# Kernel tuning notes

Hardware: AMD Instinct MI355X
Metric: run time of the kernel (lower is better)

The kernel has to match this reference:

```python
import jax, jax.numpy as jnp
import numpy as np

B, CH, H, W = 1, 128, 160, 224


def _lrelu(x):
    return jax.nn.leaky_relu(x, 0.01)


def _conv(x, w, b):
    # 1x1 conv: x [B,Cin,H,W], w [Cout,Cin], b [Cout]
    return jnp.einsum('bchw,oc->bohw', x, w) + b[None, :, None, None]


def _cmul(x, inds, Wt, b):
    # CondMul: x [N,Cin], inds [N] int32, Wt [classes,Cin,Cout], b [classes,Cout]
    return jnp.einsum('ni,nio->no', x, jnp.take(Wt, inds, axis=0)) + jnp.take(b, inds, axis=0)


def _forward(x_in, bb1_w, bb1_b, bb2_w, bb2_b, bb3_w, bb3_b,
             msk1_w, msk1_b, msk2_w, msk2_b, msk3_w, msk3_b,
             c10_w, c10_b, c20_w, c20_b, c30_w, c30_b,
             c11_W, c11_b, c21_W, c21_b, c31_W, c31_b,
             c12_W, c12_b, c22_W, c22_b, c32_W, c32_b,
             r1_w, r1_b, r2_W, r2_b, r3_W, r3_b):
    Bb, C, Hh, Ww = x_in.shape
    # backbone (1x1 convs)
    x = _lrelu(_conv(x_in, bb1_w, bb1_b))
    x = _lrelu(_conv(x, bb2_w, bb2_b))
    feat = _lrelu(_conv(x, bb3_w, bb3_b))  # [B,128,H,W]
    # mask head (note: torch applies leaky_relu to msk3 output too)
    m = _lrelu(_conv(x_in, msk1_w, msk1_b))
    m = _lrelu(_conv(m, msk2_w, msk2_b))
    mask = _lrelu(_conv(m, msk3_w, msk3_b))  # [B,1,H,W]
    # stage 1: dense classification over classes[0]=16
    y = _lrelu(_conv(feat, c10_w, c10_b))
    y = _lrelu(_conv(y, c20_w, c20_b))
    y = _conv(y, c30_w, c30_b)  # [B,16,H,W], no relu
    inds1 = jnp.argmax(y, axis=1).reshape(-1).astype(jnp.int32)  # [N], (b,h,w) order
    x_l = jnp.transpose(feat, (0, 2, 3, 1)).reshape(-1, feat.shape[1])  # [N,128]
    # stage 2: CondMul routed by inds1 (16 classes), out = 16+2*8 = 32
    t = _lrelu(_cmul(x_l, inds1, c11_W, c11_b))
    t = _lrelu(_cmul(t, inds1, c21_W, c21_b))
    t = _cmul(t, inds1, c31_W, c31_b)
    inds2 = jnp.argmax(t, axis=1).astype(jnp.int32)
    inds12 = jnp.clip(inds1 * 16 + (inds2 - 8), 0, 255).astype(jnp.int32)
    # stage 3: CondMul routed by inds12 (256 classes)
    t = _lrelu(_cmul(x_l, inds12, c12_W, c12_b))
    t = _lrelu(_cmul(t, inds12, c22_W, c22_b))
    t = _cmul(t, inds12, c32_W, c32_b)
    inds3 = jnp.argmax(t, axis=1).astype(jnp.int32)
    inds123 = jnp.clip(inds12 * 16 + (inds3 - 8), 0, 4095).astype(jnp.int32)  # classes123-1
    inds_super = inds123 // 512  # class_factor = 4096/8
    xr = _lrelu(_conv(x_in, r1_w, r1_b))
    xr_l = jnp.transpose(xr, (0, 2, 3, 1)).reshape(-1, xr.shape[1])  # [N,128]
    t = _lrelu(_cmul(xr_l, inds_super, r2_W, r2_b))
    r = _cmul(t, inds123, r3_W, r3_b).reshape(-1)
    out = ((inds123.astype(jnp.float32) + r) * (1.0 / 4096.0)).reshape(Bb, 1, Hh, Ww)
    return out, mask


def setup_inputs():
    ks = jax.random.split(jax.random.key(0), 40)
    ctr = iter(range(40))

    def p(shape, scale=0.05):
        return jax.random.normal(ks[next(ctr)], shape, dtype=jnp.float32) * scale

    d = {
        'x_in': p((B, CH, H, W), 1.0),
        'bb1_w': p((128, 128)), 'bb1_b': p((128,)),
        'bb2_w': p((128, 128)), 'bb2_b': p((128,)),
        'bb3_w': p((128, 128)), 'bb3_b': p((128,)),
        'msk1_w': p((32, 128)), 'msk1_b': p((32,)),
        'msk2_w': p((16, 32)), 'msk2_b': p((16,)),
        'msk3_w': p((1, 16)), 'msk3_b': p((1,)),
        'c10_w': p((32, 128)), 'c10_b': p((32,)),
        'c20_w': p((32, 32)), 'c20_b': p((32,)),
        'c30_w': p((16, 32)), 'c30_b': p((16,)),
        'c11_W': p((16, 128, 32)), 'c11_b': p((16, 32)),
        'c21_W': p((16, 32, 32)), 'c21_b': p((16, 32)),
        'c31_W': p((16, 32, 32)), 'c31_b': p((16, 32)),
        'c12_W': p((256, 128, 32)), 'c12_b': p((256, 32)),
        'c22_W': p((256, 32, 32)), 'c22_b': p((256, 32)),
        'c32_W': p((256, 32, 32)), 'c32_b': p((256, 32)),
        'r1_w': p((128, 128)), 'r1_b': p((128,)),
        'r2_W': p((8, 128, 32)), 'r2_b': p((8, 32)),
        'r3_W': p((4096, 32, 1)), 'r3_b': p((4096, 1)),
    }
    return d


def reference(x_in, bb1_w, bb1_b, bb2_w, bb2_b, bb3_w, bb3_b,
              msk1_w, msk1_b, msk2_w, msk2_b, msk3_w, msk3_b,
              c10_w, c10_b, c20_w, c20_b, c30_w, c30_b,
              c11_W, c11_b, c21_W, c21_b, c31_W, c31_b,
              c12_W, c12_b, c22_W, c22_b, c32_W, c32_b,
              r1_w, r1_b, r2_W, r2_b, r3_W, r3_b):
    return _forward(x_in, bb1_w, bb1_b, bb2_w, bb2_b, bb3_w, bb3_b,
                    msk1_w, msk1_b, msk2_w, msk2_b, msk3_w, msk3_b,
                    c10_w, c10_b, c20_w, c20_b, c30_w, c30_b,
                    c11_W, c11_b, c21_W, c21_b, c31_W, c31_b,
                    c12_W, c12_b, c22_W, c22_b, c32_W, c32_b,
                    r1_w, r1_b, r2_W, r2_b, r3_W, r3_b)
```

## Files before the change

### kernel.cpp

```cpp
#include <hip/hip_runtime.h>

#define N_PIX (160*224)
#define ORDER_CAP (396*256)
#define CHUNK_CAP 512
#define G_S2 156
#define G_S3 396
#define G_RG 148
#define NB   70
#define BCHUNK 512

__device__ __forceinline__ float lrelu(float v) { return v >= 0.f ? v : 0.01f * v; }

template<int CHW>
__global__ __launch_bounds__(512) void dense128_k(const float* __restrict__ in,
    const float* __restrict__ W, const float* __restrict__ b,
    float* __restrict__ out, int N)
{
  __shared__ float Wl[128*128];
  const int tid = threadIdx.x;
#pragma unroll
  for (int k = 0; k < 8; ++k)
    ((float4*)Wl)[k*512 + tid] = ((const float4*)W)[k*512 + tid];
  const int lane = tid & 63;
  const int wv = tid >> 6;
  const int ob = wv * 16;
  const int p0 = blockIdx.x * 128 + lane;
  const int p1 = p0 + 64;
  float acc0[16], acc1[16];
#pragma unroll
  for (int o = 0; o < 16; ++o) { acc0[o] = b[ob + o]; acc1[o] = acc0[o]; }
  __syncthreads();
  const float* x0 = CHW ? (in + p0) : (in + (size_t)p0 * 128);
  const float* x1 = CHW ? (in + p1) : (in + (size_t)p1 * 128);
  for (int c0 = 0; c0 < 128; c0 += 8) {
    float xa[8], xb[8];
    if (CHW) {
#pragma unroll
      for (int k = 0; k < 8; ++k) {
        xa[k] = x0[(size_t)(c0 + k) * N];
        xb[k] = x1[(size_t)(c0 + k) * N];
      }
    } else {
      float4 a0 = *(const float4*)(x0 + c0), a1 = *(const float4*)(x0 + c0 + 4);
      float4 b0 = *(const float4*)(x1 + c0), b1 = *(const float4*)(x1 + c0 + 4);
      xa[0]=a0.x; xa[1]=a0.y; xa[2]=a0.z; xa[3]=a0.w;
      xa[4]=a1.x; xa[5]=a1.y; xa[6]=a1.z; xa[7]=a1.w;
      xb[0]=b0.x; xb[1]=b0.y; xb[2]=b0.z; xb[3]=b0.w;
      xb[4]=b1.x; xb[5]=b1.y; xb[6]=b1.z; xb[7]=b1.w;
    }
#pragma unroll
    for (int o = 0; o < 16; ++o) {
      const float* wr = &Wl[(ob + o)*128 + c0];
      float4 w0 = *(const float4*)wr;
      float4 w1 = *(const float4*)(wr + 4);
      acc0[o] += xa[0]*w0.x + xa[1]*w0.y + xa[2]*w0.z + xa[3]*w0.w
               + xa[4]*w1.x + xa[5]*w1.y + xa[6]*w1.z + xa[7]*w1.w;
      acc1[o] += xb[0]*w0.x + xb[1]*w0.y + xb[2]*w0.z + xb[3]*w0.w
               + xb[4]*w1.x + xb[5]*w1.y + xb[6]*w1.z + xb[7]*w1.w;
    }
  }
  __syncthreads();
  float4* o0 = (float4*)(out + (size_t)p0 * 128 + ob);
  float4* o1 = (float4*)(out + (size_t)p1 * 128 + ob);
#pragma unroll
  for (int q = 0; q < 4; ++q) {
    o0[q] = make_float4(lrelu(acc0[4*q+0]), lrelu(acc0[4*q+1]),
                        lrelu(acc0[4*q+2]), lrelu(acc0[4*q+3]));
    o1[q] = make_float4(lrelu(acc1[4*q+0]), lrelu(acc1[4*q+1]),
                        lrelu(acc1[4*q+2]), lrelu(acc1[4*q+3]));
  }
}

__global__ __launch_bounds__(256) void mask_k(const float* __restrict__ xg,
    const float* __restrict__ W1, const float* __restrict__ b1,
    const float* __restrict__ W2, const float* __restrict__ b2,
    const float* __restrict__ W3, const float* __restrict__ b3,
    float* __restrict__ outm, int N)
{
  __shared__ float W1l[32*128], W2l[16*32], W3l[16];
  const int tid = threadIdx.x;
#pragma unroll
  for (int k = 0; k < 4; ++k)
    ((float4*)W1l)[k*256 + tid] = ((const float4*)W1)[k*256 + tid];
  if (tid < 128) ((float4*)W2l)[tid] = ((const float4*)W2)[tid];
  if (tid < 4)   ((float4*)W3l)[tid] = ((const float4*)W3)[tid];
  __syncthreads();
  const int p = blockIdx.x * 256 + tid;
  float a1[32];
#pragma unroll
  for (int o = 0; o < 32; ++o) a1[o] = b1[o];
  for (int c0 = 0; c0 < 128; c0 += 8) {
    float xs[8];
#pragma unroll
    for (int k = 0; k < 8; ++k) xs[k] = xg[(size_t)(c0 + k) * N + p];
#pragma unroll
    for (int o = 0; o < 32; ++o) {
      const float* wr = &W1l[o*128 + c0];
      float4 w0 = *(const float4*)wr, w1 = *(const float4*)(wr + 4);
      a1[o] += xs[0]*w0.x + xs[1]*w0.y + xs[2]*w0.z + xs[3]*w0.w
             + xs[4]*w1.x + xs[5]*w1.y + xs[6]*w1.z + xs[7]*w1.w;
    }
  }
#pragma unroll
  for (int o = 0; o < 32; ++o) a1[o] = lrelu(a1[o]);
  float a2[16];
#pragma unroll
  for (int o = 0; o < 16; ++o) a2[o] = b2[o];
#pragma unroll
  for (int i = 0; i < 32; i += 4) {
#pragma unroll
    for (int o = 0; o < 16; ++o) {
      float4 w = *(const float4*)&W2l[o*32 + i];
      a2[o] += a1[i]*w.x + a1[i+1]*w.y + a1[i+2]*w.z + a1[i+3]*w.w;
    }
  }
#pragma unroll
  for (int o = 0; o < 16; ++o) a2[o] = lrelu(a2[o]);
  float a3 = b3[0];
#pragma unroll
  for (int i = 0; i < 16; i += 4) {
    float4 w = *(const float4*)&W3l[i];
    a3 += a2[i]*w.x + a2[i+1]*w.y + a2[i+2]*w.z + a2[i+3]*w.w;
  }
  outm[p] = lrelu(a3);
}

__global__ __launch_bounds__(256) void stage1_k(const float* __restrict__ feat,
    const float* __restrict__ W1, const float* __restrict__ b1,
    const float* __restrict__ W2, const float* __restrict__ b2,
    const float* __restrict__ W3, const float* __restrict__ b3,
    int* __restrict__ inds1, int* __restrict__ blkcnt, int N)
{
  __shared__ float W1l[32*128], W2l[32*32], W3l[16*32];
  __shared__ int hist[16];
  const int tid = threadIdx.x;
#pragma unroll
  for (int k = 0; k < 4; ++k)
    ((float4*)W1l)[k*256 + tid] = ((const float4*)W1)[k*256 + tid];
  ((float4*)W2l)[tid] = ((const float4*)W2)[tid];
  if (tid < 128) ((float4*)W3l)[tid] = ((const float4*)W3)[tid];
  if (tid < 16) hist[tid] = 0;
  __syncthreads();
  const int p = blockIdx.x * 256 + tid;
  const float* x = feat + (size_t)p * 128;
  float a1[32];
#pragma unroll
  for (int o = 0; o < 32; ++o) a1[o] = b1[o];
  for (int c0 = 0; c0 < 128; c0 += 8) {
    float4 xa = *(const float4*)(x + c0);
    float4 xb = *(const float4*)(x + c0 + 4);
    float xs[8] = {xa.x, xa.y, xa.z, xa.w, xb.x, xb.y, xb.z, xb.w};
#pragma unroll
    for (int o = 0; o < 32; ++o) {
      const float* wr = &W1l[o*128 + c0];
      float4 w0 = *(const float4*)wr, w1 = *(const float4*)(wr + 4);
      a1[o] += xs[0]*w0.x + xs[1]*w0.y + xs[2]*w0.z + xs[3]*w0.w
             + xs[4]*w1.x + xs[5]*w1.y + xs[6]*w1.z + xs[7]*w1.w;
    }
  }
#pragma unroll
  for (int o = 0; o < 32; ++o) a1[o] = lrelu(a1[o]);
  float a2[32];
#pragma unroll
  for (int o = 0; o < 32; ++o) a2[o] = b2[o];
#pragma unroll
  for (int i = 0; i < 32; i += 4) {
#pragma unroll
    for (int o = 0; o < 32; ++o) {
      float4 w = *(const float4*)&W2l[o*32 + i];
      a2[o] += a1[i]*w.x + a1[i+1]*w.y + a1[i+2]*w.z + a1[i+3]*w.w;
    }
  }
#pragma unroll
  for (int o = 0; o < 32; ++o) a2[o] = lrelu(a2[o]);
  float lg[16];
#pragma unroll
  for (int o = 0; o < 16; ++o) lg[o] = b3[o];
#pragma unroll
  for (int i = 0; i < 32; i += 4) {
#pragma unroll
    for (int o = 0; o < 16; ++o) {
      float4 w = *(const float4*)&W3l[o*32 + i];
      lg[o] += a2[i]*w.x + a2[i+1]*w.y + a2[i+2]*w.z + a2[i+3]*w.w;
    }
  }
  float bv = lg[0]; int bi = 0;
#pragma unroll
  for (int o = 1; o < 16; ++o) if (lg[o] > bv) { bv = lg[o]; bi = o; }
  inds1[p] = bi;
  atomicAdd(&hist[bi], 1);
  __syncthreads();
  if (tid < 16) blkcnt[blockIdx.x * 16 + tid] = hist[tid];
}

__global__ __launch_bounds__(256) void stage23_k(const float* __restrict__ act,
    const float* __restrict__ W1g, const float* __restrict__ b1g,
    const float* __restrict__ W2g, const float* __restrict__ b2g,
    const float* __restrict__ W3g, const float* __restrict__ b3g,
    const int* __restrict__ chunk_class, const int* __restrict__ order,
    const int* __restrict__ offs_this, const int* __restrict__ cnts_this,
    int* __restrict__ out_ind, int hi)
{
  const int cls = chunk_class[blockIdx.x];
  if (cls < 0) return;
  __shared__ float W1l[128*32], W2l[32*32], W3l[32*32];
  __shared__ float b1l[32], b2l[32], b3l[32];
  const int tid = threadIdx.x;
  const float* W1 = W1g + (size_t)cls * 4096;
  const float* W2 = W2g + (size_t)cls * 1024;
  const float* W3 = W3g + (size_t)cls * 1024;
#pragma unroll
  for (int k = 0; k < 4; ++k)
    ((float4*)W1l)[k*256 + tid] = ((const float4*)W1)[k*256 + tid];
  ((float4*)W2l)[tid] = ((const float4*)W2)[tid];
  ((float4*)W3l)[tid] = ((const float4*)W3)[tid];
  if (tid < 32) {
    b1l[tid] = b1g[cls*32 + tid];
    b2l[tid] = b2g[cls*32 + tid];
    b3l[tid] = b3g[cls*32 + tid];
  }
  const int slot = blockIdx.x * 256 + tid;
  const int end = offs_this[cls] + cnts_this[cls];
  __syncthreads();
  if (slot >= end) return;
  const int p = order[slot];
  const float* x = act + (size_t)p * 128;
  float a1[32];
#pragma unroll
  for (int o = 0; o < 32; ++o) a1[o] = b1l[o];
  for (int i0 = 0; i0 < 128; i0 += 8) {
    float4 xa = *(const float4*)(x + i0);
    float4 xb = *(const float4*)(x + i0 + 4);
    float xs[8] = {xa.x, xa.y, xa.z, xa.w, xb.x, xb.y, xb.z, xb.w};
#pragma unroll
    for (int i = 0; i < 8; ++i) {
#pragma unroll
      for (int o4 = 0; o4 < 8; ++o4) {
        float4 w = *(const float4*)&W1l[(i0 + i)*32 + o4*4];
        a1[o4*4+0] += xs[i]*w.x; a1[o4*4+1] += xs[i]*w.y;
        a1[o4*4+2] += xs[i]*w.z; a1[o4*4+3] += xs[i]*w.w;
      }
    }
  }
#pragma unroll
  for (int o = 0; o < 32; ++o) a1[o] = lrelu(a1[o]);
  float a2[32];
#pragma unroll
  for (int o = 0; o < 32; ++o) a2[o] = b2l[o];
#pragma unroll
  for (int i = 0; i < 32; ++i) {
#pragma unroll
    for (int o4 = 0; o4 < 8; ++o4) {
      float4 w = *(const float4*)&W2l[i*32 + o4*4];
      a2[o4*4+0] += a1[i]*w.x; a2[o4*4+1] += a1[i]*w.y;
      a2[o4*4+2] += a1[i]*w.z; a2[o4*4+3] += a1[i]*w.w;
    }
  }
#pragma unroll
  for (int o = 0; o < 32; ++o) a2[o] = lrelu(a2[o]);
  float a3[32];
#pragma unroll
  for (int o = 0; o < 32; ++o) a3[o] = b3l[o];
#pragma unroll
  for (int i = 0; i < 32; ++i) {
#pragma unroll
    for (int o4 = 0; o4 < 8; ++o4) {
      float4 w = *(const float4*)&W3l[i*32 + o4*4];
      a3[o4*4+0] += a2[i]*w.x; a3[o4*4+1] += a2[i]*w.y;
      a3[o4*4+2] += a2[i]*w.z; a3[o4*4+3] += a2[i]*w.w;
    }
  }
  float bv = a3[0]; int bi = 0;
#pragma unroll
  for (int o = 1; o < 32; ++o) if (a3[o] > bv) { bv = a3[o]; bi = o; }
  int v = cls*16 + bi - 8;
  v = v < 0 ? 0 : (v > hi ? hi : v);
  out_ind[p] = v;
}

__global__ __launch_bounds__(256) void reg_k(const float* __restrict__ act,
    const float* __restrict__ W1g, const float* __restrict__ b1g,
    const float* __restrict__ r3W, const float* __restrict__ r3b,
    const int* __restrict__ chunk_class, const int* __restrict__ order,
    const int* __restrict__ offs_this, const int* __restrict__ cnts_this,
    const int* __restrict__ inds123, float* __restrict__ outr)
{
  const int cls = chunk_class[blockIdx.x];
  if (cls < 0) return;
  __shared__ float W1l[128*32], b1l[32];
  const int tid = threadIdx.x;
  const float* W1 = W1g + (size_t)cls * 4096;
#pragma unroll
  for (int k = 0; k < 4; ++k)
    ((float4*)W1l)[k*256 + tid] = ((const float4*)W1)[k*256 + tid];
  if (tid < 32) b1l[tid] = b1g[cls*32 + tid];
  const int slot = blockIdx.x * 256 + tid;
  const int end = offs_this[cls] + cnts_this[cls];
  __syncthreads();
  if (slot >= end) return;
  const int p = order[slot];
  const float* x = act + (size_t)p * 128;
  float a1[32];
#pragma unroll
  for (int o = 0; o < 32; ++o) a1[o] = b1l[o];
  for (int i0 = 0; i0 < 128; i0 += 8) {
    float4 xa = *(const float4*)(x + i0);
    float4 xb = *(const float4*)(x + i0 + 4);
    float xs[8] = {xa.x, xa.y, xa.z, xa.w, xb.x, xb.y, xb.z, xb.w};
#pragma unroll
    for (int i = 0; i < 8; ++i) {
#pragma unroll
      for (int o4 = 0; o4 < 8; ++o4) {
        float4 w = *(const float4*)&W1l[(i0 + i)*32 + o4*4];
        a1[o4*4+0] += xs[i]*w.x; a1[o4*4+1] += xs[i]*w.y;
        a1[o4*4+2] += xs[i]*w.z; a1[o4*4+3] += xs[i]*w.w;
      }
    }
  }
#pragma unroll
  for (int o = 0; o < 32; ++o) a1[o] = lrelu(a1[o]);
  const int ind = inds123[p];
  const float4* rw = (const float4*)(r3W + (size_t)ind * 32);
  float r = r3b[ind];
#pragma unroll
  for (int k = 0; k < 8; ++k) {
    float4 w = rw[k];
    r += a1[4*k+0]*w.x + a1[4*k+1]*w.y + a1[4*k+2]*w.z + a1[4*k+3]*w.w;
  }
  outr[p] = ((float)ind + r) * (1.0f / 4096.0f);
}

__global__ __launch_bounds__(256) void hist_k(const int* __restrict__ ind,
    int* __restrict__ blkcnt, int shift, int C)
{
  __shared__ int h[256];
  const int tid = threadIdx.x, b = blockIdx.x;
  h[tid] = 0;
  __syncthreads();
  const int base = b * BCHUNK;
  atomicAdd(&h[ind[base + tid] >> shift], 1);
  atomicAdd(&h[ind[base + 256 + tid] >> shift], 1);
  __syncthreads();
  if (tid < C) blkcnt[b * C + tid] = h[tid];
}

__global__ __launch_bounds__(256) void scan_k(const int* __restrict__ blkcnt,
    int* __restrict__ blkbase, int* __restrict__ offsets, int* __restrict__ counts,
    int* __restrict__ chunk_class, int C, int fillTo, int nb)
{
  __shared__ int cl[256], ol[256];
  __shared__ int totChunks;
  const int tid = threadIdx.x;
  if (tid < C) {
    int s = 0;
    for (int b = 0; b < nb; ++b) s += blkcnt[b * C + tid];
    cl[tid] = s;
  }
  __syncthreads();
  if (tid == 0) {
    int off = 0;
    for (int c = 0; c < C; ++c) {
      ol[c] = off;
      off += ((cl[c] + 255) >> 8) << 8;
    }
    totChunks = off >> 8;
  }
  __syncthreads();
  if (tid < C) {
    offsets[tid] = ol[tid];
    counts[tid]  = cl[tid];
    int acc = ol[tid];
    for (int b = 0; b < nb; ++b) {
      int v = blkcnt[b * C + tid];
      blkbase[b * C + tid] = acc;
      acc += v;
    }
    const int start = ol[tid] >> 8;
    const int nch = (cl[tid] + 255) >> 8;
    for (int k = 0; k < nch; ++k) chunk_class[start + k] = tid;
  }
  for (int k = totChunks + tid; k < fillTo; k += 256) chunk_class[k] = -1;
}

__global__ __launch_bounds__(256) void scatter_k(const int* __restrict__ ind,
    const int* __restrict__ blkbase, int* __restrict__ order, int shift, int C,
    int chunkpx)
{
  __shared__ int lcur[256], lbase[256];
  const int tid = threadIdx.x, b = blockIdx.x;
  lcur[tid] = 0;
  if (tid < C) lbase[tid] = blkbase[b * C + tid];
  __syncthreads();
  const int base = b * chunkpx;
  for (int r = 0; r < chunkpx; r += 256) {
    const int p = base + r + tid;
    const int c = ind[p] >> shift;
    const int rank = atomicAdd(&lcur[c], 1);
    order[lbase[c] + rank] = p;
  }
}

extern "C" void kernel_launch(void* const* d_in, const int* in_sizes, int n_in,
                              void* d_out, int out_size, void* d_ws, size_t ws_size,
                              hipStream_t stream)
{
  const int N = N_PIX;
  const float* x_in  = (const float*)d_in[0];
  const float* bb1_w = (const float*)d_in[1];  const float* bb1_b = (const float*)d_in[2];
  const float* bb2_w = (const float*)d_in[3];  const float* bb2_b = (const float*)d_in[4];
  const float* bb3_w = (const float*)d_in[5];  const float* bb3_b = (const float*)d_in[6];
  const float* msk1_w= (const float*)d_in[7];  const float* msk1_b= (const float*)d_in[8];
  const float* msk2_w= (const float*)d_in[9];  const float* msk2_b= (const float*)d_in[10];
  const float* msk3_w= (const float*)d_in[11]; const float* msk3_b= (const float*)d_in[12];
  const float* c10_w = (const float*)d_in[13]; const float* c10_b = (const float*)d_in[14];
  const float* c20_w = (const float*)d_in[15]; const float* c20_b = (const float*)d_in[16];
  const float* c30_w = (const float*)d_in[17]; const float* c30_b = (const float*)d_in[18];
  const float* c11_W = (const float*)d_in[19]; const float* c11_b = (const float*)d_in[20];
  const float* c21_W = (const float*)d_in[21]; const float* c21_b = (const float*)d_in[22];
  const float* c31_W = (const float*)d_in[23]; const float* c31_b = (const float*)d_in[24];
  const float* c12_W = (const float*)d_in[25]; const float* c12_b = (const float*)d_in[26];
  const float* c22_W = (const float*)d_in[27]; const float* c22_b = (const float*)d_in[28];
  const float* c32_W = (const float*)d_in[29]; const float* c32_b = (const float*)d_in[30];
  const float* r1_w  = (const float*)d_in[31]; const float* r1_b  = (const float*)d_in[32];
  const float* r2_W  = (const float*)d_in[33]; const float* r2_b  = (const float*)d_in[34];
  const float* r3_W  = (const float*)d_in[35]; const float* r3_b  = (const float*)d_in[36];

  float* act     = (float*)d_ws;
  int*   inds1   = (int*)(act + (size_t)N * 128);
  int*   inds12  = inds1 + N;
  int*   inds123 = inds12 + N;
  int*   counts  = inds123 + N;
  int*   offs    = counts + 256;
  int*   chunk_cls = offs + 256;
  int*   order     = chunk_cls + CHUNK_CAP;
  int*   blkcnt    = order + ORDER_CAP;
  int*   blkbase   = blkcnt + 70*256;

  float* out_reg  = (float*)d_out;
  float* out_mask = out_reg + N;

  const dim3 B(256);
  const dim3 B512(512);
  const int gDense  = N / 128;
  const int gPix256 = N / 256;

  dense128_k<1><<<gDense, B512, 0, stream>>>(x_in, bb1_w, bb1_b, act, N);
  dense128_k<0><<<gDense, B512, 0, stream>>>(act,  bb2_w, bb2_b, act, N);
  dense128_k<0><<<gDense, B512, 0, stream>>>(act,  bb3_w, bb3_b, act, N);

  mask_k<<<gPix256, B, 0, stream>>>(x_in, msk1_w, msk1_b, msk2_w, msk2_b,
                                    msk3_w, msk3_b, out_mask, N);

  stage1_k<<<gPix256, B, 0, stream>>>(act, c10_w, c10_b, c20_w, c20_b,
                                      c30_w, c30_b, inds1, blkcnt, N);

  scan_k<<<1, B, 0, stream>>>(blkcnt, blkbase, offs, counts, chunk_cls, 16, G_S2, 140);
  scatter_k<<<140, B, 0, stream>>>(inds1, blkbase, order, 0, 16, 256);
  stage23_k<<<G_S2, B, 0, stream>>>(act, c11_W, c11_b, c21_W, c21_b, c31_W, c31_b,
                                    chunk_cls, order, offs, counts, inds12, 255);

  hist_k<<<NB, B, 0, stream>>>(inds12, blkcnt, 0, 256);
  scan_k<<<1, B, 0, stream>>>(blkcnt, blkbase, offs, counts, chunk_cls, 256, G_S3, NB);
  scatter_k<<<NB, B, 0, stream>>>(inds12, blkbase, order, 0, 256, BCHUNK);
  stage23_k<<<G_S3, B, 0, stream>>>(act, c12_W, c12_b, c22_W, c22_b, c32_W, c32_b,
                                    chunk_cls, order, offs, counts, inds123, 4095);

  dense128_k<1><<<gDense, B512, 0, stream>>>(x_in, r1_w, r1_b, act, N);

  hist_k<<<NB, B, 0, stream>>>(inds123, blkcnt, 9, 8);
  scan_k<<<1, B, 0, stream>>>(blkcnt, blkbase, offs, counts, chunk_cls, 8, G_RG, NB);
  scatter_k<<<NB, B, 0, stream>>>(inds123, blkbase, order, 9, 8, BCHUNK);
  reg_k<<<G_RG, B, 0, stream>>>(act, r2_W, r2_b, r3_W, r3_b,
                                chunk_cls, order, offs, counts, inds123, out_reg);
}
```

Before: 533.4 us.

## Split dense 1x1 convs across output halves and shrink per-pixel kernel blocks

The dense 128x128 conv kernel is templated on output count so each block computes only 64 output channels, which doubles the grid and halves the shared-memory weight tile. Ping-pong activation buffers are added in the workspace so that the split blocks never read and write the same buffer in place. The mask and stage1 kernels and the first scatter move to 128-thread blocks with twice as many blocks, to fill the GPU better. The cost is that each input activation is now read twice (once per half), and the workspace must be larger; if it is too small, the code falls back to the old 128-output path.

```diff
diff --git a/kernel.cpp b/kernel.cpp
--- a/kernel.cpp
+++ b/kernel.cpp
@@ -11,24 +11,29 @@
 
 __device__ __forceinline__ float lrelu(float v) { return v >= 0.f ? v : 0.01f * v; }
 
-template<int CHW>
+template<int CHW, int OUTS>
 __global__ __launch_bounds__(512) void dense128_k(const float* __restrict__ in,
     const float* __restrict__ W, const float* __restrict__ b,
     float* __restrict__ out, int N)
 {
-  __shared__ float Wl[128*128];
-  const int tid = threadIdx.x;
-#pragma unroll
-  for (int k = 0; k < 8; ++k)
-    ((float4*)Wl)[k*512 + tid] = ((const float4*)W)[k*512 + tid];
+  __shared__ float Wl[OUTS*128];
+  const int tid = threadIdx.x;
+  const int half = (OUTS == 128) ? 0 : (blockIdx.x & 1);
+  const int pblk = (OUTS == 128) ? blockIdx.x : (blockIdx.x >> 1);
+  const float4* Wg = ((const float4*)W) + half * (OUTS * 32);
+#pragma unroll
+  for (int k = 0; k < OUTS*128/2048; ++k)
+    ((float4*)Wl)[k*512 + tid] = Wg[k*512 + tid];
   const int lane = tid & 63;
   const int wv = tid >> 6;
-  const int ob = wv * 16;
-  const int p0 = blockIdx.x * 128 + lane;
+  constexpr int WO = OUTS / 8;
+  const int ob  = wv * WO;
+  const int obg = half * OUTS + ob;
+  const int p0 = pblk * 128 + lane;
   const int p1 = p0 + 64;
-  float acc0[16], acc1[16];
-#pragma unroll
-  for (int o = 0; o < 16; ++o) { acc0[o] = b[ob + o]; acc1[o] = acc0[o]; }
+  float acc0[WO], acc1[WO];
+#pragma unroll
+  for (int o = 0; o < WO; ++o) { acc0[o] = b[obg + o]; acc1[o] = acc0[o]; }
   __syncthreads();
   const float* x0 = CHW ? (in + p0) : (in + (size_t)p0 * 128);
   const float* x1 = CHW ? (in + p1) : (in + (size_t)p1 * 128);
@@ -49,7 +54,7 @@
       xb[4]=b1.x; xb[5]=b1.y; xb[6]=b1.z; xb[7]=b1.w;
     }
 #pragma unroll
-    for (int o = 0; o < 16; ++o) {
+    for (int o = 0; o < WO; ++o) {
       const float* wr = &Wl[(ob + o)*128 + c0];
       float4 w0 = *(const float4*)wr;
       float4 w1 = *(const float4*)(wr + 4);
@@ -60,10 +65,10 @@
     }
   }
   __syncthreads();
-  float4* o0 = (float4*)(out + (size_t)p0 * 128 + ob);
-  float4* o1 = (float4*)(out + (size_t)p1 * 128 + ob);
-#pragma unroll
-  for (int q = 0; q < 4; ++q) {
+  float4* o0 = (float4*)(out + (size_t)p0 * 128 + obg);
+  float4* o1 = (float4*)(out + (size_t)p1 * 128 + obg);
+#pragma unroll
+  for (int q = 0; q < WO/4; ++q) {
     o0[q] = make_float4(lrelu(acc0[4*q+0]), lrelu(acc0[4*q+1]),
                         lrelu(acc0[4*q+2]), lrelu(acc0[4*q+3]));
     o1[q] = make_float4(lrelu(acc1[4*q+0]), lrelu(acc1[4*q+1]),
@@ -71,7 +76,7 @@
   }
 }
 
-__global__ __launch_bounds__(256) void mask_k(const float* __restrict__ xg,
+__global__ __launch_bounds__(128) void mask_k(const float* __restrict__ xg,
     const float* __restrict__ W1, const float* __restrict__ b1,
     const float* __restrict__ W2, const float* __restrict__ b2,
     const float* __restrict__ W3, const float* __restrict__ b3,
@@ -80,12 +85,12 @@
   __shared__ float W1l[32*128], W2l[16*32], W3l[16];
   const int tid = threadIdx.x;
 #pragma unroll
-  for (int k = 0; k < 4; ++k)
-    ((float4*)W1l)[k*256 + tid] = ((const float4*)W1)[k*256 + tid];
-  if (tid < 128) ((float4*)W2l)[tid] = ((const float4*)W2)[tid];
-  if (tid < 4)   ((float4*)W3l)[tid] = ((const float4*)W3)[tid];
-  __syncthreads();
-  const int p = blockIdx.x * 256 + tid;
+  for (int k = 0; k < 8; ++k)
+    ((float4*)W1l)[k*128 + tid] = ((const float4*)W1)[k*128 + tid];
+  ((float4*)W2l)[tid] = ((const float4*)W2)[tid];
+  if (tid < 4) ((float4*)W3l)[tid] = ((const float4*)W3)[tid];
+  __syncthreads();
+  const int p = blockIdx.x * 128 + tid;
   float a1[32];
 #pragma unroll
   for (int o = 0; o < 32; ++o) a1[o] = b1[o];
@@ -125,7 +130,7 @@
   outm[p] = lrelu(a3);
 }
 
-__global__ __launch_bounds__(256) void stage1_k(const float* __restrict__ feat,
+__global__ __launch_bounds__(128) void stage1_k(const float* __restrict__ feat,
     const float* __restrict__ W1, const float* __restrict__ b1,
     const float* __restrict__ W2, const float* __restrict__ b2,
     const float* __restrict__ W3, const float* __restrict__ b3,
@@ -135,13 +140,15 @@
   __shared__ int hist[16];
   const int tid = threadIdx.x;
 #pragma unroll
-  for (int k = 0; k < 4; ++k)
-    ((float4*)W1l)[k*256 + tid] = ((const float4*)W1)[k*256 + tid];
-  ((float4*)W2l)[tid] = ((const float4*)W2)[tid];
-  if (tid < 128) ((float4*)W3l)[tid] = ((const float4*)W3)[tid];
+  for (int k = 0; k < 8; ++k)
+    ((float4*)W1l)[k*128 + tid] = ((const float4*)W1)[k*128 + tid];
+#pragma unroll
+  for (int k = 0; k < 2; ++k)
+    ((float4*)W2l)[k*128 + tid] = ((const float4*)W2)[k*128 + tid];
+  ((float4*)W3l)[tid] = ((const float4*)W3)[tid];
   if (tid < 16) hist[tid] = 0;
   __syncthreads();
-  const int p = blockIdx.x * 256 + tid;
+  const int p = blockIdx.x * 128 + tid;
   const float* x = feat + (size_t)p * 128;
   float a1[32];
 #pragma unroll
@@ -382,18 +389,18 @@
   for (int k = totChunks + tid; k < fillTo; k += 256) chunk_class[k] = -1;
 }
 
-__global__ __launch_bounds__(256) void scatter_k(const int* __restrict__ ind,
+__global__ void scatter_k(const int* __restrict__ ind,
     const int* __restrict__ blkbase, int* __restrict__ order, int shift, int C,
     int chunkpx)
 {
   __shared__ int lcur[256], lbase[256];
   const int tid = threadIdx.x, b = blockIdx.x;
-  lcur[tid] = 0;
+  if (tid < 256) lcur[tid] = 0;
   if (tid < C) lbase[tid] = blkbase[b * C + tid];
   __syncthreads();
   const int base = b * chunkpx;
-  for (int r = 0; r < chunkpx; r += 256) {
-    const int p = base + r + tid;
+  for (int r = tid; r < chunkpx; r += blockDim.x) {
+    const int p = base + r;
     const int c = ind[p] >> shift;
     const int rank = atomicAdd(&lcur[c], 1);
     order[lbase[c] + rank] = p;
@@ -425,8 +432,7 @@
   const float* r2_W  = (const float*)d_in[33]; const float* r2_b  = (const float*)d_in[34];
   const float* r3_W  = (const float*)d_in[35]; const float* r3_b  = (const float*)d_in[36];
 
-  float* act     = (float*)d_ws;
-  int*   inds1   = (int*)(act + (size_t)N * 128);
+  int*   inds1   = (int*)d_ws;
   int*   inds12  = inds1 + N;
   int*   inds123 = inds12 + N;
   int*   counts  = inds123 + N;
@@ -435,27 +441,39 @@
   int*   order     = chunk_cls + CHUNK_CAP;
   int*   blkcnt    = order + ORDER_CAP;
   int*   blkbase   = blkcnt + 70*256;
+  const size_t intWords = 3*(size_t)N + 512 + CHUNK_CAP + ORDER_CAP + 2*70*256;
+  float* act  = (float*)((int*)d_ws + intWords);
+  const size_t need = intWords*4 + 2*(size_t)N*128*4;
+  const bool halved = ws_size >= need;
+  float* act2 = halved ? (act + (size_t)N*128) : act;
 
   float* out_reg  = (float*)d_out;
   float* out_mask = out_reg + N;
 
   const dim3 B(256);
+  const dim3 B128(128);
   const dim3 B512(512);
-  const int gDense  = N / 128;
-  const int gPix256 = N / 256;
-
-  dense128_k<1><<<gDense, B512, 0, stream>>>(x_in, bb1_w, bb1_b, act, N);
-  dense128_k<0><<<gDense, B512, 0, stream>>>(act,  bb2_w, bb2_b, act, N);
-  dense128_k<0><<<gDense, B512, 0, stream>>>(act,  bb3_w, bb3_b, act, N);
-
-  mask_k<<<gPix256, B, 0, stream>>>(x_in, msk1_w, msk1_b, msk2_w, msk2_b,
-                                    msk3_w, msk3_b, out_mask, N);
-
-  stage1_k<<<gPix256, B, 0, stream>>>(act, c10_w, c10_b, c20_w, c20_b,
-                                      c30_w, c30_b, inds1, blkcnt, N);
-
-  scan_k<<<1, B, 0, stream>>>(blkcnt, blkbase, offs, counts, chunk_cls, 16, G_S2, 140);
-  scatter_k<<<140, B, 0, stream>>>(inds1, blkbase, order, 0, 16, 256);
+  const int gPix128 = N / 128;
+  const int gDenseH = 2 * gPix128;
+
+  if (halved) {
+    dense128_k<1,64><<<gDenseH, B512, 0, stream>>>(x_in, bb1_w, bb1_b, act,  N);
+    dense128_k<0,64><<<gDenseH, B512, 0, stream>>>(act,  bb2_w, bb2_b, act2, N);
+    dense128_k<0,64><<<gDenseH, B512, 0, stream>>>(act2, bb3_w, bb3_b, act,  N);
+  } else {
+    dense128_k<1,128><<<gPix128, B512, 0, stream>>>(x_in, bb1_w, bb1_b, act, N);
+    dense128_k<0,128><<<gPix128, B512, 0, stream>>>(act,  bb2_w, bb2_b, act, N);
+    dense128_k<0,128><<<gPix128, B512, 0, stream>>>(act,  bb3_w, bb3_b, act, N);
+  }
+
+  mask_k<<<gPix128, B128, 0, stream>>>(x_in, msk1_w, msk1_b, msk2_w, msk2_b,
+                                       msk3_w, msk3_b, out_mask, N);
+
+  stage1_k<<<gPix128, B128, 0, stream>>>(act, c10_w, c10_b, c20_w, c20_b,
+                                         c30_w, c30_b, inds1, blkcnt, N);
+
+  scan_k<<<1, B, 0, stream>>>(blkcnt, blkbase, offs, counts, chunk_cls, 16, G_S2, 280);
+  scatter_k<<<280, B128, 0, stream>>>(inds1, blkbase, order, 0, 16, 128);
   stage23_k<<<G_S2, B, 0, stream>>>(act, c11_W, c11_b, c21_W, c21_b, c31_W, c31_b,
                                     chunk_cls, order, offs, counts, inds12, 255);
 
@@ -465,11 +483,16 @@
   stage23_k<<<G_S3, B, 0, stream>>>(act, c12_W, c12_b, c22_W, c22_b, c32_W, c32_b,
                                     chunk_cls, order, offs, counts, inds123, 4095);
 
-  dense128_k<1><<<gDense, B512, 0, stream>>>(x_in, r1_w, r1_b, act, N);
+  float* xr = halved ? act2 : act;
+  if (halved) {
+    dense128_k<1,64><<<gDenseH, B512, 0, stream>>>(x_in, r1_w, r1_b, act2, N);
+  } else {
+    dense128_k<1,128><<<gPix128, B512, 0, stream>>>(x_in, r1_w, r1_b, act, N);
+  }
 
   hist_k<<<NB, B, 0, stream>>>(inds123, blkcnt, 9, 8);
   scan_k<<<1, B, 0, stream>>>(blkcnt, blkbase, offs, counts, chunk_cls, 8, G_RG, NB);
   scatter_k<<<NB, B, 0, stream>>>(inds123, blkbase, order, 9, 8, BCHUNK);
-  reg_k<<<G_RG, B, 0, stream>>>(act, r2_W, r2_b, r3_W, r3_b,
+  reg_k<<<G_RG, B, 0, stream>>>(xr, r2_W, r2_b, r3_W, r3_b,
                                 chunk_cls, order, offs, counts, inds123, out_reg);
 }
```

Result: slower. 617.3 us (+15.7%).
